# Kernel optimization log

Hardware: AMD Instinct MI355X
Metric: run time of the kernel (lower is better)

## Reference

```python
import jax, jax.numpy as jnp
import numpy as np

H = 128
N_ATOMS = 20000
N_BONDS = 60000
BATCH = 8


def _linear_params(key, fan_in, fan_out, bias=True):
    kw, kb = jax.random.split(key)
    lim = 1.0 / np.sqrt(fan_in)
    W = jax.random.uniform(kw, (fan_in, fan_out), jnp.float32, -lim, lim)
    if bias:
        b = jax.random.uniform(kb, (fan_out,), jnp.float32, -lim, lim)
        return W, b
    return W


def setup_inputs() -> dict:
    key = jax.random.key(0)
    ks = jax.random.split(key, 12)
    h = jax.random.normal(ks[0], (BATCH, N_ATOMS, H), jnp.float32)
    x = jax.random.normal(ks[1], (BATCH, N_ATOMS, 3), jnp.float32)
    bond_indices = jax.random.randint(ks[2], (N_BONDS, 2), 0, N_ATOMS, jnp.int64)
    Wm1, bm1 = _linear_params(ks[3], 2 * H + 1, H)
    Wm2, bm2 = _linear_params(ks[4], H, H)
    Wn1, bn1 = _linear_params(ks[5], 2 * H, H)
    Wn2, bn2 = _linear_params(ks[6], H, H)
    Wc1, bc1 = _linear_params(ks[7], H, H)
    # xavier_uniform gain=0.001 for final coord layer [1, H] in torch -> [H, 1] here
    lim = 0.001 * np.sqrt(6.0 / (H + 1))
    Wc2 = jax.random.uniform(ks[8], (H, 1), jnp.float32, -lim, lim)
    return dict(h=h, x=x, bond_indices=bond_indices,
                Wm1=Wm1, bm1=bm1, Wm2=Wm2, bm2=bm2,
                Wn1=Wn1, bn1=bn1, Wn2=Wn2, bn2=bn2,
                Wc1=Wc1, bc1=bc1, Wc2=Wc2)


def reference(h, x, bond_indices, Wm1, bm1, Wm2, bm2, Wn1, bn1, Wn2, bn2, Wc1, bc1, Wc2):
    silu = jax.nn.silu
    n_atoms = h.shape[1]
    src = bond_indices[:, 0]
    dst = bond_indices[:, 1]

    h_src = h[:, src, :]            # [B, E, H]
    h_dst = h[:, dst, :]
    coord_diff = x[:, dst, :] - x[:, src, :]   # [B, E, 3]
    dist = jnp.linalg.norm(coord_diff, axis=-1, keepdims=True)  # [B, E, 1]

    mi = jnp.concatenate([h_src, h_dst, dist], axis=-1)  # [B, E, 2H+1]
    messages = silu(silu(mi @ Wm1 + bm1) @ Wm2 + bm2)    # [B, E, H]

    aggregated = jnp.zeros_like(h).at[:, dst, :].add(messages).at[:, src, :].add(messages)

    h_in = jnp.concatenate([h, aggregated], axis=-1)     # [B, N, 2H]
    h_out = h + (silu(h_in @ Wn1 + bn1) @ Wn2 + bn2)

    coord_weights = silu(messages @ Wc1 + bc1) @ Wc2     # [B, E, 1]
    coord_diff_norm = coord_diff / (dist + 1e-8)
    upd = coord_diff_norm * coord_weights                # [B, E, 3]
    coord_update = jnp.zeros_like(x).at[:, dst, :].add(upd).at[:, src, :].add(-upd)

    ones = jnp.ones(src.shape[0], dtype=h.dtype)
    bond_counts = jnp.zeros(n_atoms, dtype=h.dtype).at[dst].add(ones).at[src].add(ones)
    bond_counts = jnp.clip(bond_counts, 1.0, None)
    x_out = x + coord_update / bond_counts[None, :, None]
    return h_out, x_out
```

## Files before the change

### kernel.cpp

```cpp
#include <hip/hip_runtime.h>


#define H      128
#define NA     20000
#define NB     60000
#define NBATCH 8
#define ADJ_CAP 32

typedef __bf16 bf16;
typedef __bf16 bf16x4 __attribute__((ext_vector_type(4)));
typedef __bf16 bf16x8 __attribute__((ext_vector_type(8)));
typedef float  f32x4  __attribute__((ext_vector_type(4)));

__device__ __forceinline__ float silu_f(float v) {
  float e = __expf(-v);
  return v * __builtin_amdgcn_rcpf(1.0f + e);
}

__device__ __forceinline__ int tswz(int row, int col) {
  return (row << 7) + (((((col) >> 3) ^ (row & 7)) << 3) | (col & 7));
}

__global__ void cast_h(const float* __restrict__ src, bf16* __restrict__ dst) {
  int i = blockIdx.x * 256 + threadIdx.x;
  float4 v = *(const float4*)(src + (size_t)i * 4);
  bf16x4 t = {(bf16)v.x, (bf16)v.y, (bf16)v.z, (bf16)v.w};
  *(bf16x4*)(dst + (size_t)i * 4) = t;
}

__device__ __forceinline__ void pack_one(const float* __restrict__ src,
                                         bf16* __restrict__ dst, int K,
                                         int i) {
  int k = i >> 7, n = i & 127;
  int nt = n >> 4, ks = k >> 5;
  int lane = (((k >> 3) & 3) << 4) | (n & 15);
  int j = k & 7;
  int KS = K >> 5;
  dst[((((nt * KS + ks) * 64) + lane) << 3) + j] = (bf16)src[i];
}

__global__ void pack_all(const float* __restrict__ Wm1,
                         const float* __restrict__ Wm2,
                         const float* __restrict__ Wn1,
                         const float* __restrict__ Wn2,
                         const float* __restrict__ Wc1,
                         bf16* __restrict__ W1p, bf16* __restrict__ W2p,
                         bf16* __restrict__ Wn1p, bf16* __restrict__ Wn2p,
                         bf16* __restrict__ Wc1p) {
  int i = blockIdx.x * 256 + threadIdx.x;
  if (i < 32768)       pack_one(Wm1, W1p, 256, i);
  else if (i < 49152)  pack_one(Wm2, W2p, 128, i - 32768);
  else if (i < 81920)  pack_one(Wn1, Wn1p, 256, i - 49152);
  else if (i < 98304)  pack_one(Wn2, Wn2p, 128, i - 81920);
  else if (i < 114688) pack_one(Wc1, Wc1p, 128, i - 98304);
}

__global__ void build_adj2(const int* __restrict__ bonds,
                           int* __restrict__ degI, int* __restrict__ adj2) {
  int e = blockIdx.x * 256 + threadIdx.x;
  if (e >= NB) return;
  int s = bonds[2 * e], d = bonds[2 * e + 1];
  int p = atomicAdd(&degI[s], 1);
  if (p < ADJ_CAP) adj2[s * ADJ_CAP + p] = (e << 1);
  p = atomicAdd(&degI[d], 1);
  if (p < ADJ_CAP) adj2[d * ADJ_CAP + p] = (e << 1) | 1;
}

__global__ __launch_bounds__(256, 4) void msg_kernel(
    const bf16* __restrict__ hb, const float* __restrict__ x,
    const int* __restrict__ bonds,
    const bf16* __restrict__ W1p, const float* __restrict__ bm1,
    const bf16* __restrict__ W2p, const float* __restrict__ bm2,
    const float* __restrict__ w1c,
    const bf16* __restrict__ Wc1p, const float* __restrict__ bc1,
    const float* __restrict__ Wc2,
    bf16* __restrict__ msgOut, float* __restrict__ updv) {
  __shared__ __align__(16) bf16 Tbuf[64 * 128];
  __shared__ __align__(16) float cds[64 * 3];
  __shared__ __align__(16) float dists[64];
  __shared__ __align__(16) float bm1s[128], bm2s[128], w1cs[128];
  __shared__ __align__(16) float bc1s[128], wc2s[128];
  __shared__ float cwpart[2][64];

  const int tid = threadIdx.x, blk = blockIdx.x;

  if (tid < 64) {
    int Rg = blk * 64 + tid;
    int bond = Rg >> 3, batch = Rg & 7;
    int s = bonds[2 * bond], dn = bonds[2 * bond + 1];
    const float* xs = x + (size_t)(batch * NA + s) * 3;
    const float* xd = x + (size_t)(batch * NA + dn) * 3;
    float c0 = xd[0] - xs[0], c1 = xd[1] - xs[1], c2 = xd[2] - xs[2];
    cds[tid * 3 + 0] = c0; cds[tid * 3 + 1] = c1; cds[tid * 3 + 2] = c2;
    dists[tid] = sqrtf(c0 * c0 + c1 * c1 + c2 * c2);
  }
  if (tid < 128) {
    bm1s[tid] = bm1[tid]; bm2s[tid] = bm2[tid]; w1cs[tid] = w1c[tid];
    bc1s[tid] = bc1[tid]; wc2s[tid] = Wc2[tid];
  }
  __syncthreads();

  const int lane = tid & 63;
  const int quad = lane >> 4, l16 = lane & 15;
  const int wave = tid >> 6;
  const int rowBase = (wave >> 1) * 32;
  const int colG = wave & 1;
  const int colBase = colG * 64;
  const bf16x8* W1v = (const bf16x8*)W1p;
  const bf16x8* W2v = (const bf16x8*)W2p;
  const bf16x8* Wc1v = (const bf16x8*)Wc1p;

  const int row0 = rowBase + l16, row1 = row0 + 16;
  const int Rg0 = blk * 64 + row0;
  const int bn0 = Rg0 >> 3, bat0 = Rg0 & 7;
  const bf16* hs0 = hb + (size_t)(bat0 * NA + bonds[2 * bn0]) * H;
  const bf16* hd0 = hb + (size_t)(bat0 * NA + bonds[2 * bn0 + 1]) * H;
  const int Rg1 = Rg0 + 16;
  const int bn1_ = Rg1 >> 3, bat1 = Rg1 & 7;
  const bf16* hs1 = hb + (size_t)(bat1 * NA + bonds[2 * bn1_]) * H;
  const bf16* hd1 = hb + (size_t)(bat1 * NA + bonds[2 * bn1_ + 1]) * H;
  const float dist0 = dists[row0], dist1 = dists[row1];

  f32x4 acc0[4], acc1[4];
#pragma unroll
  for (int nt = 0; nt < 4; nt++) {
    acc0[nt] = (f32x4){0.f, 0.f, 0.f, 0.f};
    acc1[nt] = (f32x4){0.f, 0.f, 0.f, 0.f};
  }

#pragma unroll
  for (int ks = 0; ks < 4; ks++) {
    bf16x8 a0 = *(const bf16x8*)(hs0 + ks * 32 + quad * 8);
    bf16x8 a1 = *(const bf16x8*)(hs1 + ks * 32 + quad * 8);
#pragma unroll
    for (int nt = 0; nt < 4; nt++) {
      bf16x8 b = W1v[((colG * 4 + nt) * 8 + ks) * 64 + lane];
      acc0[nt] = __builtin_amdgcn_mfma_f32_16x16x32_bf16(b, a0, acc0[nt], 0, 0, 0);
      acc1[nt] = __builtin_amdgcn_mfma_f32_16x16x32_bf16(b, a1, acc1[nt], 0, 0, 0);
    }
  }
#pragma unroll
  for (int ks = 4; ks < 8; ks++) {
    bf16x8 a0 = *(const bf16x8*)(hd0 + (ks - 4) * 32 + quad * 8);
    bf16x8 a1 = *(const bf16x8*)(hd1 + (ks - 4) * 32 + quad * 8);
#pragma unroll
    for (int nt = 0; nt < 4; nt++) {
      bf16x8 b = W1v[((colG * 4 + nt) * 8 + ks) * 64 + lane];
      acc0[nt] = __builtin_amdgcn_mfma_f32_16x16x32_bf16(b, a0, acc0[nt], 0, 0, 0);
      acc1[nt] = __builtin_amdgcn_mfma_f32_16x16x32_bf16(b, a1, acc1[nt], 0, 0, 0);
    }
  }
#pragma unroll
  for (int nt = 0; nt < 4; nt++) {
    int col = colBase + nt * 16 + quad * 4;
    f32x4 bb = *(const f32x4*)&bm1s[col];
    f32x4 wc = *(const f32x4*)&w1cs[col];
    bf16x4 o0, o1;
#pragma unroll
    for (int reg = 0; reg < 4; reg++) {
      o0[reg] = (bf16)silu_f(acc0[nt][reg] + bb[reg] + dist0 * wc[reg]);
      o1[reg] = (bf16)silu_f(acc1[nt][reg] + bb[reg] + dist1 * wc[reg]);
    }
    *(bf16x4*)&Tbuf[tswz(row0, col)] = o0;
    *(bf16x4*)&Tbuf[tswz(row1, col)] = o1;
  }
  __syncthreads();

#pragma unroll
  for (int nt = 0; nt < 4; nt++) {
    acc0[nt] = (f32x4){0.f, 0.f, 0.f, 0.f};
    acc1[nt] = (f32x4){0.f, 0.f, 0.f, 0.f};
  }
#pragma unroll
  for (int ks = 0; ks < 4; ks++) {
    bf16x8 a0 = *(const bf16x8*)&Tbuf[tswz(row0, ks * 32 + quad * 8)];
    bf16x8 a1 = *(const bf16x8*)&Tbuf[tswz(row1, ks * 32 + quad * 8)];
#pragma unroll
    for (int nt = 0; nt < 4; nt++) {
      bf16x8 b = W2v[((colG * 4 + nt) * 4 + ks) * 64 + lane];
      acc0[nt] = __builtin_amdgcn_mfma_f32_16x16x32_bf16(b, a0, acc0[nt], 0, 0, 0);
      acc1[nt] = __builtin_amdgcn_mfma_f32_16x16x32_bf16(b, a1, acc1[nt], 0, 0, 0);
    }
  }
  __syncthreads();
#pragma unroll
  for (int nt = 0; nt < 4; nt++) {
    int col = colBase + nt * 16 + quad * 4;
    f32x4 bb = *(const f32x4*)&bm2s[col];
    bf16x4 o0, o1;
#pragma unroll
    for (int reg = 0; reg < 4; reg++) {
      o0[reg] = (bf16)silu_f(acc0[nt][reg] + bb[reg]);
      o1[reg] = (bf16)silu_f(acc1[nt][reg] + bb[reg]);
    }
    *(bf16x4*)&Tbuf[tswz(row0, col)] = o0;
    *(bf16x4*)&Tbuf[tswz(row1, col)] = o1;
  }
  __syncthreads();

#pragma unroll
  for (int nt = 0; nt < 4; nt++) {
    acc0[nt] = (f32x4){0.f, 0.f, 0.f, 0.f};
    acc1[nt] = (f32x4){0.f, 0.f, 0.f, 0.f};
  }
#pragma unroll
  for (int ks = 0; ks < 4; ks++) {
    bf16x8 a0 = *(const bf16x8*)&Tbuf[tswz(row0, ks * 32 + quad * 8)];
    bf16x8 a1 = *(const bf16x8*)&Tbuf[tswz(row1, ks * 32 + quad * 8)];
#pragma unroll
    for (int nt = 0; nt < 4; nt++) {
      bf16x8 b = Wc1v[((colG * 4 + nt) * 4 + ks) * 64 + lane];
      acc0[nt] = __builtin_amdgcn_mfma_f32_16x16x32_bf16(b, a0, acc0[nt], 0, 0, 0);
      acc1[nt] = __builtin_amdgcn_mfma_f32_16x16x32_bf16(b, a1, acc1[nt], 0, 0, 0);
    }
  }

#pragma unroll
  for (int i = 0; i < 4; i++) {
    int item = i * 256 + tid;
    int row = item >> 4, cg = item & 15;
    *(bf16x8*)&msgOut[(size_t)(blk * 64 + row) * H + cg * 8] =
        *(const bf16x8*)&Tbuf[tswz(row, cg * 8)];
  }

  float s0 = 0.f, s1 = 0.f;
#pragma unroll
  for (int nt = 0; nt < 4; nt++) {
    int col = colBase + nt * 16 + quad * 4;
    f32x4 bb = *(const f32x4*)&bc1s[col];
    f32x4 w2 = *(const f32x4*)&wc2s[col];
#pragma unroll
    for (int reg = 0; reg < 4; reg++) {
      s0 += silu_f(acc0[nt][reg] + bb[reg]) * w2[reg];
      s1 += silu_f(acc1[nt][reg] + bb[reg]) * w2[reg];
    }
  }
  s0 += __shfl_xor(s0, 16); s0 += __shfl_xor(s0, 32);
  s1 += __shfl_xor(s1, 16); s1 += __shfl_xor(s1, 32);
  if (quad == 0) {
    cwpart[colG][row0] = s0;
    cwpart[colG][row1] = s1;
  }
  __syncthreads();
  if (colG == 0 && quad == 0) {
#pragma unroll
    for (int rs = 0; rs < 2; rs++) {
      int row = rs ? row1 : row0;
      size_t Rg = (size_t)blk * 64 + row;
      float cw = cwpart[0][row] + cwpart[1][row];
      float inv = 1.0f / (dists[row] + 1e-8f);
#pragma unroll
      for (int c = 0; c < 3; c++)
        updv[Rg * 3 + c] = cds[row * 3 + c] * inv * cw;
    }
  }
}

__global__ __launch_bounds__(256, 4) void node_kernel(
    const float* __restrict__ h, const bf16* __restrict__ hb,
    const bf16* __restrict__ msg, const float* __restrict__ updv,
    const int* __restrict__ degI, const int* __restrict__ adj2,
    const bf16* __restrict__ Wn1p, const float* __restrict__ bn1,
    const bf16* __restrict__ Wn2p, const float* __restrict__ bn2,
    const float* __restrict__ x,
    float* __restrict__ hout, float* __restrict__ xout) {
  __shared__ __align__(16) bf16 Abuf[64 * 128];
  __shared__ __align__(16) bf16 Tbuf[64 * 128];

  const int tid = threadIdx.x, blk = blockIdx.x;

  {
    const int row = tid >> 2, c4 = tid & 3;
    const int Rg = blk * 64 + row;
    const int atomA = Rg % NA, batA = Rg / NA;
    int deg = degI[atomA];
    if (deg > ADJ_CAP) deg = ADJ_CAP;
    const int* ap = adj2 + atomA * ADJ_CAP;
    float a32[32];
#pragma unroll
    for (int t = 0; t < 32; t++) a32[t] = 0.f;
    float sx = 0.f, sy = 0.f, sz = 0.f;
    int j = 0;
    for (; j + 2 <= deg; j += 2) {
      int2 e2 = *(const int2*)&ap[j];
      const bf16* m0 = msg + ((size_t)(e2.x >> 1) * 8 + batA) * H + c4 * 32;
      const bf16* m1 = msg + ((size_t)(e2.y >> 1) * 8 + batA) * H + c4 * 32;
      bf16x8 v0 = *(const bf16x8*)(m0),      v1 = *(const bf16x8*)(m0 + 8);
      bf16x8 v2 = *(const bf16x8*)(m0 + 16), v3 = *(const bf16x8*)(m0 + 24);
      bf16x8 u0 = *(const bf16x8*)(m1),      u1 = *(const bf16x8*)(m1 + 8);
      bf16x8 u2 = *(const bf16x8*)(m1 + 16), u3 = *(const bf16x8*)(m1 + 24);
      if (c4 == 0) {
        float sg0 = (e2.x & 1) ? 1.0f : -1.0f;
        float sg1 = (e2.y & 1) ? 1.0f : -1.0f;
        const float* uv0 = updv + ((size_t)(e2.x >> 1) * 8 + batA) * 3;
        const float* uv1 = updv + ((size_t)(e2.y >> 1) * 8 + batA) * 3;
        sx += sg0 * uv0[0] + sg1 * uv1[0];
        sy += sg0 * uv0[1] + sg1 * uv1[1];
        sz += sg0 * uv0[2] + sg1 * uv1[2];
      }
#pragma unroll
      for (int t = 0; t < 8; t++) {
        a32[t]      += (float)v0[t] + (float)u0[t];
        a32[8 + t]  += (float)v1[t] + (float)u1[t];
        a32[16 + t] += (float)v2[t] + (float)u2[t];
        a32[24 + t] += (float)v3[t] + (float)u3[t];
      }
    }
    if (j < deg) {
      int ent0 = ap[j];
      const bf16* m0 = msg + ((size_t)(ent0 >> 1) * 8 + batA) * H + c4 * 32;
      if (c4 == 0) {
        float sg0 = (ent0 & 1) ? 1.0f : -1.0f;
        const float* uv0 = updv + ((size_t)(ent0 >> 1) * 8 + batA) * 3;
        sx += sg0 * uv0[0]; sy += sg0 * uv0[1]; sz += sg0 * uv0[2];
      }
#pragma unroll
      for (int k = 0; k < 4; k++) {
        bf16x8 v = *(const bf16x8*)(m0 + 8 * k);
#pragma unroll
        for (int t = 0; t < 8; t++) a32[8 * k + t] += (float)v[t];
      }
    }
    if (c4 == 0) {
      float cnt = deg < 1 ? 1.0f : (float)deg;
      float inv = 1.0f / cnt;
      size_t o = (size_t)Rg * 3;
      xout[o + 0] = x[o + 0] + sx * inv;
      xout[o + 1] = x[o + 1] + sy * inv;
      xout[o + 2] = x[o + 2] + sz * inv;
    }
#pragma unroll
    for (int k = 0; k < 4; k++) {
      bf16x8 w;
#pragma unroll
      for (int t = 0; t < 8; t++) w[t] = (bf16)a32[8 * k + t];
      *(bf16x8*)&Abuf[tswz(row, c4 * 32 + 8 * k)] = w;
    }
  }
  __syncthreads();

  const int lane = tid & 63, wave = tid >> 6;
  const int quad = lane >> 4, l16 = lane & 15;
  const int rowBase = (wave >> 1) * 32, colG = wave & 1, colBase = colG * 64;
  const int row0 = rowBase + l16, row1 = row0 + 16;
  const size_t RgA0 = (size_t)blk * 64 + row0;
  const size_t RgA1 = RgA0 + 16;
  const bf16* hrow0 = hb + RgA0 * H;
  const bf16* hrow1 = hb + RgA1 * H;
  const bf16x8* W1v = (const bf16x8*)Wn1p;
  const bf16x8* W2v = (const bf16x8*)Wn2p;

  f32x4 acc0[4], acc1[4];
#pragma unroll
  for (int nt = 0; nt < 4; nt++) {
    acc0[nt] = (f32x4){0.f, 0.f, 0.f, 0.f};
    acc1[nt] = (f32x4){0.f, 0.f, 0.f, 0.f};
  }

#pragma unroll
  for (int ks = 0; ks < 4; ks++) {
    bf16x8 a0 = *(const bf16x8*)(hrow0 + ks * 32 + quad * 8);
    bf16x8 a1 = *(const bf16x8*)(hrow1 + ks * 32 + quad * 8);
#pragma unroll
    for (int nt = 0; nt < 4; nt++) {
      bf16x8 b = W1v[((colG * 4 + nt) * 8 + ks) * 64 + lane];
      acc0[nt] = __builtin_amdgcn_mfma_f32_16x16x32_bf16(b, a0, acc0[nt], 0, 0, 0);
      acc1[nt] = __builtin_amdgcn_mfma_f32_16x16x32_bf16(b, a1, acc1[nt], 0, 0, 0);
    }
  }
#pragma unroll
  for (int ks2 = 0; ks2 < 4; ks2++) {
    bf16x8 a0 = *(const bf16x8*)&Abuf[tswz(row0, ks2 * 32 + quad * 8)];
    bf16x8 a1 = *(const bf16x8*)&Abuf[tswz(row1, ks2 * 32 + quad * 8)];
#pragma unroll
    for (int nt = 0; nt < 4; nt++) {
      bf16x8 b = W1v[((colG * 4 + nt) * 8 + 4 + ks2) * 64 + lane];
      acc0[nt] = __builtin_amdgcn_mfma_f32_16x16x32_bf16(b, a0, acc0[nt], 0, 0, 0);
      acc1[nt] = __builtin_amdgcn_mfma_f32_16x16x32_bf16(b, a1, acc1[nt], 0, 0, 0);
    }
  }
#pragma unroll
  for (int nt = 0; nt < 4; nt++) {
    int col = colBase + nt * 16 + quad * 4;
    f32x4 bb = *(const f32x4*)&bn1[col];
    bf16x4 o0, o1;
#pragma unroll
    for (int reg = 0; reg < 4; reg++) {
      o0[reg] = (bf16)silu_f(acc0[nt][reg] + bb[reg]);
      o1[reg] = (bf16)silu_f(acc1[nt][reg] + bb[reg]);
    }
    *(bf16x4*)&Tbuf[tswz(row0, col)] = o0;
    *(bf16x4*)&Tbuf[tswz(row1, col)] = o1;
  }
  __syncthreads();

#pragma unroll
  for (int nt = 0; nt < 4; nt++) {
    acc0[nt] = (f32x4){0.f, 0.f, 0.f, 0.f};
    acc1[nt] = (f32x4){0.f, 0.f, 0.f, 0.f};
  }
#pragma unroll
  for (int ks = 0; ks < 4; ks++) {
    bf16x8 a0 = *(const bf16x8*)&Tbuf[tswz(row0, ks * 32 + quad * 8)];
    bf16x8 a1 = *(const bf16x8*)&Tbuf[tswz(row1, ks * 32 + quad * 8)];
#pragma unroll
    for (int nt = 0; nt < 4; nt++) {
      bf16x8 b = W2v[((colG * 4 + nt) * 4 + ks) * 64 + lane];
      acc0[nt] = __builtin_amdgcn_mfma_f32_16x16x32_bf16(b, a0, acc0[nt], 0, 0, 0);
      acc1[nt] = __builtin_amdgcn_mfma_f32_16x16x32_bf16(b, a1, acc1[nt], 0, 0, 0);
    }
  }
#pragma unroll
  for (int nt = 0; nt < 4; nt++) {
    int col = colBase + nt * 16 + quad * 4;
    f32x4 bb = *(const f32x4*)&bn2[col];
    f32x4 hv0 = *(const f32x4*)&h[RgA0 * H + col];
    f32x4 hv1 = *(const f32x4*)&h[RgA1 * H + col];
    f32x4 o0, o1;
#pragma unroll
    for (int reg = 0; reg < 4; reg++) {
      o0[reg] = hv0[reg] + acc0[nt][reg] + bb[reg];
      o1[reg] = hv1[reg] + acc1[nt][reg] + bb[reg];
    }
    *(f32x4*)&hout[RgA0 * H + col] = o0;
    *(f32x4*)&hout[RgA1 * H + col] = o1;
  }
}

extern "C" void kernel_launch(void* const* d_in, const int* in_sizes, int n_in,
                              void* d_out, int out_size, void* d_ws,
                              size_t ws_size, hipStream_t stream) {
  const float* h    = (const float*)d_in[0];
  const float* x    = (const float*)d_in[1];
  const int*  bonds = (const int*)d_in[2];
  const float* Wm1  = (const float*)d_in[3];
  const float* bm1  = (const float*)d_in[4];
  const float* Wm2  = (const float*)d_in[5];
  const float* bm2  = (const float*)d_in[6];
  const float* Wn1  = (const float*)d_in[7];
  const float* bn1  = (const float*)d_in[8];
  const float* Wn2  = (const float*)d_in[9];
  const float* bn2  = (const float*)d_in[10];
  const float* Wc1  = (const float*)d_in[11];
  const float* bc1  = (const float*)d_in[12];
  const float* Wc2  = (const float*)d_in[13];

  float* out  = (float*)d_out;
  float* hout = out;
  float* xout = out + (size_t)NBATCH * NA * H;

  char* ws = (char*)d_ws;
  const size_t OFF_DEG  = 0;
  const size_t OFF_W1   = 163840;
  const size_t OFF_W2   = OFF_W1 + 65536;
  const size_t OFF_WN1  = OFF_W2 + 32768;
  const size_t OFF_WN2  = OFF_WN1 + 65536;
  const size_t OFF_WC1  = OFF_WN2 + 32768;
  const size_t OFF_ADJ2 = 393216;
  const size_t OFF_UPDV = 2953216;
  const size_t OFF_HB   = 8713216;
  const size_t OFF_MSG  = 49673216;

  int*   degI = (int*)(ws + OFF_DEG);
  bf16*  W1p  = (bf16*)(ws + OFF_W1);
  bf16*  W2p  = (bf16*)(ws + OFF_W2);
  bf16*  Wn1p = (bf16*)(ws + OFF_WN1);
  bf16*  Wn2p = (bf16*)(ws + OFF_WN2);
  bf16*  Wc1p = (bf16*)(ws + OFF_WC1);
  int*   adj2 = (int*)(ws + OFF_ADJ2);
  float* updv = (float*)(ws + OFF_UPDV);
  bf16*  hb   = (bf16*)(ws + OFF_HB);
  bf16*  msgB = (bf16*)(ws + OFF_MSG);

  (void)hipMemsetAsync(degI, 0, NA * sizeof(int), stream);

  cast_h<<<NBATCH * NA * H / 1024, 256, 0, stream>>>(h, hb);
  pack_all<<<448, 256, 0, stream>>>(Wm1, Wm2, Wn1, Wn2, Wc1,
                                    W1p, W2p, Wn1p, Wn2p, Wc1p);
  build_adj2<<<(NB + 255) / 256, 256, 0, stream>>>(bonds, degI, adj2);

  msg_kernel<<<NB * NBATCH / 64, 256, 0, stream>>>(
      hb, x, bonds, W1p, bm1, W2p, bm2, Wm1 + 256 * H, Wc1p, bc1, Wc2,
      msgB, updv);
  node_kernel<<<NBATCH * NA / 64, 256, 0, stream>>>(
      h, hb, msgB, updv, degI, adj2, Wn1p, bn1, Wn2p, bn2, x,
      hout, xout);
}
```

Baseline: 433.0 us.

## Merge prep kernels into one launch and enlarge message tile to 96 rows

The three preprocessing kernels (cast h to bf16, pack weights, build adjacency) are fused into a single kernel that dispatches on block index, saving two launches. The message kernel now handles 96 edge-rows per block instead of 64, with each wave computing three 16-row MFMA fragments rather than two. This reuses each loaded weight fragment across more rows. In exchange it uses more accumulator registers and LDS, which may lower occupancy under the 4-blocks launch bound.

```diff
diff --git a/kernel.cpp b/kernel.cpp
--- a/kernel.cpp
+++ b/kernel.cpp
@@ -19,13 +19,6 @@
 
 __device__ __forceinline__ int tswz(int row, int col) {
   return (row << 7) + (((((col) >> 3) ^ (row & 7)) << 3) | (col & 7));
-}
-
-__global__ void cast_h(const float* __restrict__ src, bf16* __restrict__ dst) {
-  int i = blockIdx.x * 256 + threadIdx.x;
-  float4 v = *(const float4*)(src + (size_t)i * 4);
-  bf16x4 t = {(bf16)v.x, (bf16)v.y, (bf16)v.z, (bf16)v.w};
-  *(bf16x4*)(dst + (size_t)i * 4) = t;
 }
 
 __device__ __forceinline__ void pack_one(const float* __restrict__ src,
@@ -39,31 +32,43 @@
   dst[((((nt * KS + ks) * 64) + lane) << 3) + j] = (bf16)src[i];
 }
 
-__global__ void pack_all(const float* __restrict__ Wm1,
-                         const float* __restrict__ Wm2,
-                         const float* __restrict__ Wn1,
-                         const float* __restrict__ Wn2,
-                         const float* __restrict__ Wc1,
-                         bf16* __restrict__ W1p, bf16* __restrict__ W2p,
-                         bf16* __restrict__ Wn1p, bf16* __restrict__ Wn2p,
-                         bf16* __restrict__ Wc1p) {
-  int i = blockIdx.x * 256 + threadIdx.x;
-  if (i < 32768)       pack_one(Wm1, W1p, 256, i);
-  else if (i < 49152)  pack_one(Wm2, W2p, 128, i - 32768);
-  else if (i < 81920)  pack_one(Wn1, Wn1p, 256, i - 49152);
-  else if (i < 98304)  pack_one(Wn2, Wn2p, 128, i - 81920);
-  else if (i < 114688) pack_one(Wc1, Wc1p, 128, i - 98304);
-}
-
-__global__ void build_adj2(const int* __restrict__ bonds,
-                           int* __restrict__ degI, int* __restrict__ adj2) {
-  int e = blockIdx.x * 256 + threadIdx.x;
-  if (e >= NB) return;
-  int s = bonds[2 * e], d = bonds[2 * e + 1];
-  int p = atomicAdd(&degI[s], 1);
-  if (p < ADJ_CAP) adj2[s * ADJ_CAP + p] = (e << 1);
-  p = atomicAdd(&degI[d], 1);
-  if (p < ADJ_CAP) adj2[d * ADJ_CAP + p] = (e << 1) | 1;
+#define PREP_CAST_BLKS 20000
+#define PREP_PACK_BLKS 448
+#define PREP_ADJ_BLKS  235
+__global__ void prep_kernel(const float* __restrict__ h, bf16* __restrict__ hb,
+                            const float* __restrict__ Wm1,
+                            const float* __restrict__ Wm2,
+                            const float* __restrict__ Wn1,
+                            const float* __restrict__ Wn2,
+                            const float* __restrict__ Wc1,
+                            bf16* __restrict__ W1p, bf16* __restrict__ W2p,
+                            bf16* __restrict__ Wn1p, bf16* __restrict__ Wn2p,
+                            bf16* __restrict__ Wc1p,
+                            const int* __restrict__ bonds,
+                            int* __restrict__ degI, int* __restrict__ adj2) {
+  const int blk = blockIdx.x;
+  if (blk < PREP_CAST_BLKS) {
+    int i = blk * 256 + threadIdx.x;
+    float4 v = *(const float4*)(h + (size_t)i * 4);
+    bf16x4 t = {(bf16)v.x, (bf16)v.y, (bf16)v.z, (bf16)v.w};
+    *(bf16x4*)(hb + (size_t)i * 4) = t;
+  } else if (blk < PREP_CAST_BLKS + PREP_PACK_BLKS) {
+    int i = (blk - PREP_CAST_BLKS) * 256 + threadIdx.x;
+    if (i < 32768)       pack_one(Wm1, W1p, 256, i);
+    else if (i < 49152)  pack_one(Wm2, W2p, 128, i - 32768);
+    else if (i < 81920)  pack_one(Wn1, Wn1p, 256, i - 49152);
+    else if (i < 98304)  pack_one(Wn2, Wn2p, 128, i - 81920);
+    else if (i < 114688) pack_one(Wc1, Wc1p, 128, i - 98304);
+  } else {
+    int e = (blk - PREP_CAST_BLKS - PREP_PACK_BLKS) * 256 + threadIdx.x;
+    if (e < NB) {
+      int s = bonds[2 * e], d = bonds[2 * e + 1];
+      int p = atomicAdd(&degI[s], 1);
+      if (p < ADJ_CAP) adj2[s * ADJ_CAP + p] = (e << 1);
+      p = atomicAdd(&degI[d], 1);
+      if (p < ADJ_CAP) adj2[d * ADJ_CAP + p] = (e << 1) | 1;
+    }
+  }
 }
 
 __global__ __launch_bounds__(256, 4) void msg_kernel(
@@ -75,17 +80,17 @@
     const bf16* __restrict__ Wc1p, const float* __restrict__ bc1,
     const float* __restrict__ Wc2,
     bf16* __restrict__ msgOut, float* __restrict__ updv) {
-  __shared__ __align__(16) bf16 Tbuf[64 * 128];
-  __shared__ __align__(16) float cds[64 * 3];
-  __shared__ __align__(16) float dists[64];
+  __shared__ __align__(16) bf16 Tbuf[96 * 128];
+  __shared__ __align__(16) float cds[96 * 3];
+  __shared__ __align__(16) float dists[96];
   __shared__ __align__(16) float bm1s[128], bm2s[128], w1cs[128];
   __shared__ __align__(16) float bc1s[128], wc2s[128];
-  __shared__ float cwpart[2][64];
+  __shared__ float cwpart[2][96];
 
   const int tid = threadIdx.x, blk = blockIdx.x;
 
-  if (tid < 64) {
-    int Rg = blk * 64 + tid;
+  if (tid < 96) {
+    int Rg = blk * 96 + tid;
     int bond = Rg >> 3, batch = Rg & 7;
     int s = bonds[2 * bond], dn = bonds[2 * bond + 1];
     const float* xs = x + (size_t)(batch * NA + s) * 3;
@@ -103,15 +108,15 @@
   const int lane = tid & 63;
   const int quad = lane >> 4, l16 = lane & 15;
   const int wave = tid >> 6;
-  const int rowBase = (wave >> 1) * 32;
+  const int rowBase = (wave >> 1) * 48;
   const int colG = wave & 1;
   const int colBase = colG * 64;
   const bf16x8* W1v = (const bf16x8*)W1p;
   const bf16x8* W2v = (const bf16x8*)W2p;
   const bf16x8* Wc1v = (const bf16x8*)Wc1p;
 
-  const int row0 = rowBase + l16, row1 = row0 + 16;
-  const int Rg0 = blk * 64 + row0;
+  const int row0 = rowBase + l16, row1 = row0 + 16, row2 = row0 + 32;
+  const int Rg0 = blk * 96 + row0;
   const int bn0 = Rg0 >> 3, bat0 = Rg0 & 7;
   const bf16* hs0 = hb + (size_t)(bat0 * NA + bonds[2 * bn0]) * H;
   const bf16* hd0 = hb + (size_t)(bat0 * NA + bonds[2 * bn0 + 1]) * H;
@@ -119,35 +124,44 @@
   const int bn1_ = Rg1 >> 3, bat1 = Rg1 & 7;
   const bf16* hs1 = hb + (size_t)(bat1 * NA + bonds[2 * bn1_]) * H;
   const bf16* hd1 = hb + (size_t)(bat1 * NA + bonds[2 * bn1_ + 1]) * H;
-  const float dist0 = dists[row0], dist1 = dists[row1];
-
-  f32x4 acc0[4], acc1[4];
+  const int Rg2 = Rg0 + 32;
+  const int bn2_ = Rg2 >> 3, bat2 = Rg2 & 7;
+  const bf16* hs2 = hb + (size_t)(bat2 * NA + bonds[2 * bn2_]) * H;
+  const bf16* hd2 = hb + (size_t)(bat2 * NA + bonds[2 * bn2_ + 1]) * H;
+  const float dist0 = dists[row0], dist1 = dists[row1], dist2 = dists[row2];
+
+  f32x4 acc0[4], acc1[4], acc2[4];
 #pragma unroll
   for (int nt = 0; nt < 4; nt++) {
     acc0[nt] = (f32x4){0.f, 0.f, 0.f, 0.f};
     acc1[nt] = (f32x4){0.f, 0.f, 0.f, 0.f};
+    acc2[nt] = (f32x4){0.f, 0.f, 0.f, 0.f};
   }
 
 #pragma unroll
   for (int ks = 0; ks < 4; ks++) {
     bf16x8 a0 = *(const bf16x8*)(hs0 + ks * 32 + quad * 8);
     bf16x8 a1 = *(const bf16x8*)(hs1 + ks * 32 + quad * 8);
+    bf16x8 a2 = *(const bf16x8*)(hs2 + ks * 32 + quad * 8);
 #pragma unroll
     for (int nt = 0; nt < 4; nt++) {
       bf16x8 b = W1v[((colG * 4 + nt) * 8 + ks) * 64 + lane];
       acc0[nt] = __builtin_amdgcn_mfma_f32_16x16x32_bf16(b, a0, acc0[nt], 0, 0, 0);
       acc1[nt] = __builtin_amdgcn_mfma_f32_16x16x32_bf16(b, a1, acc1[nt], 0, 0, 0);
+      acc2[nt] = __builtin_amdgcn_mfma_f32_16x16x32_bf16(b, a2, acc2[nt], 0, 0, 0);
     }
   }
 #pragma unroll
   for (int ks = 4; ks < 8; ks++) {
     bf16x8 a0 = *(const bf16x8*)(hd0 + (ks - 4) * 32 + quad * 8);
     bf16x8 a1 = *(const bf16x8*)(hd1 + (ks - 4) * 32 + quad * 8);
+    bf16x8 a2 = *(const bf16x8*)(hd2 + (ks - 4) * 32 + quad * 8);
 #pragma unroll
     for (int nt = 0; nt < 4; nt++) {
       bf16x8 b = W1v[((colG * 4 + nt) * 8 + ks) * 64 + lane];
       acc0[nt] = __builtin_amdgcn_mfma_f32_16x16x32_bf16(b, a0, acc0[nt], 0, 0, 0);
       acc1[nt] = __builtin_amdgcn_mfma_f32_16x16x32_bf16(b, a1, acc1[nt], 0, 0, 0);
+      acc2[nt] = __builtin_amdgcn_mfma_f32_16x16x32_bf16(b, a2, acc2[nt], 0, 0, 0);
     }
   }
 #pragma unroll
@@ -155,14 +169,16 @@
     int col = colBase + nt * 16 + quad * 4;
     f32x4 bb = *(const f32x4*)&bm1s[col];
     f32x4 wc = *(const f32x4*)&w1cs[col];
-    bf16x4 o0, o1;
+    bf16x4 o0, o1, o2;
 #pragma unroll
     for (int reg = 0; reg < 4; reg++) {
       o0[reg] = (bf16)silu_f(acc0[nt][reg] + bb[reg] + dist0 * wc[reg]);
       o1[reg] = (bf16)silu_f(acc1[nt][reg] + bb[reg] + dist1 * wc[reg]);
+      o2[reg] = (bf16)silu_f(acc2[nt][reg] + bb[reg] + dist2 * wc[reg]);
     }
     *(bf16x4*)&Tbuf[tswz(row0, col)] = o0;
     *(bf16x4*)&Tbuf[tswz(row1, col)] = o1;
+    *(bf16x4*)&Tbuf[tswz(row2, col)] = o2;
   }
   __syncthreads();
 
@@ -170,16 +186,19 @@
   for (int nt = 0; nt < 4; nt++) {
     acc0[nt] = (f32x4){0.f, 0.f, 0.f, 0.f};
     acc1[nt] = (f32x4){0.f, 0.f, 0.f, 0.f};
+    acc2[nt] = (f32x4){0.f, 0.f, 0.f, 0.f};
   }
 #pragma unroll
   for (int ks = 0; ks < 4; ks++) {
     bf16x8 a0 = *(const bf16x8*)&Tbuf[tswz(row0, ks * 32 + quad * 8)];
     bf16x8 a1 = *(const bf16x8*)&Tbuf[tswz(row1, ks * 32 + quad * 8)];
+    bf16x8 a2 = *(const bf16x8*)&Tbuf[tswz(row2, ks * 32 + quad * 8)];
 #pragma unroll
     for (int nt = 0; nt < 4; nt++) {
       bf16x8 b = W2v[((colG * 4 + nt) * 4 + ks) * 64 + lane];
       acc0[nt] = __builtin_amdgcn_mfma_f32_16x16x32_bf16(b, a0, acc0[nt], 0, 0, 0);
       acc1[nt] = __builtin_amdgcn_mfma_f32_16x16x32_bf16(b, a1, acc1[nt], 0, 0, 0);
+      acc2[nt] = __builtin_amdgcn_mfma_f32_16x16x32_bf16(b, a2, acc2[nt], 0, 0, 0);
     }
   }
   __syncthreads();
@@ -187,14 +206,16 @@
   for (int nt = 0; nt < 4; nt++) {
     int col = colBase + nt * 16 + quad * 4;
     f32x4 bb = *(const f32x4*)&bm2s[col];
-    bf16x4 o0, o1;
+    bf16x4 o0, o1, o2;
 #pragma unroll
     for (int reg = 0; reg < 4; reg++) {
       o0[reg] = (bf16)silu_f(acc0[nt][reg] + bb[reg]);
       o1[reg] = (bf16)silu_f(acc1[nt][reg] + bb[reg]);
+      o2[reg] = (bf16)silu_f(acc2[nt][reg] + bb[reg]);
     }
     *(bf16x4*)&Tbuf[tswz(row0, col)] = o0;
     *(bf16x4*)&Tbuf[tswz(row1, col)] = o1;
+    *(bf16x4*)&Tbuf[tswz(row2, col)] = o2;
   }
   __syncthreads();
 
@@ -202,28 +223,31 @@
   for (int nt = 0; nt < 4; nt++) {
     acc0[nt] = (f32x4){0.f, 0.f, 0.f, 0.f};
     acc1[nt] = (f32x4){0.f, 0.f, 0.f, 0.f};
+    acc2[nt] = (f32x4){0.f, 0.f, 0.f, 0.f};
   }
 #pragma unroll
   for (int ks = 0; ks < 4; ks++) {
     bf16x8 a0 = *(const bf16x8*)&Tbuf[tswz(row0, ks * 32 + quad * 8)];
     bf16x8 a1 = *(const bf16x8*)&Tbuf[tswz(row1, ks * 32 + quad * 8)];
+    bf16x8 a2 = *(const bf16x8*)&Tbuf[tswz(row2, ks * 32 + quad * 8)];
 #pragma unroll
     for (int nt = 0; nt < 4; nt++) {
       bf16x8 b = Wc1v[((colG * 4 + nt) * 4 + ks) * 64 + lane];
       acc0[nt] = __builtin_amdgcn_mfma_f32_16x16x32_bf16(b, a0, acc0[nt], 0, 0, 0);
       acc1[nt] = __builtin_amdgcn_mfma_f32_16x16x32_bf16(b, a1, acc1[nt], 0, 0, 0);
-    }
-  }
-
-#pragma unroll
-  for (int i = 0; i < 4; i++) {
+      acc2[nt] = __builtin_amdgcn_mfma_f32_16x16x32_bf16(b, a2, acc2[nt], 0, 0, 0);
+    }
+  }
+
+#pragma unroll
+  for (int i = 0; i < 6; i++) {
     int item = i * 256 + tid;
     int row = item >> 4, cg = item & 15;
-    *(bf16x8*)&msgOut[(size_t)(blk * 64 + row) * H + cg * 8] =
+    *(bf16x8*)&msgOut[(size_t)(blk * 96 + row) * H + cg * 8] =
         *(const bf16x8*)&Tbuf[tswz(row, cg * 8)];
   }
 
-  float s0 = 0.f, s1 = 0.f;
+  float s0 = 0.f, s1 = 0.f, s2 = 0.f;
 #pragma unroll
   for (int nt = 0; nt < 4; nt++) {
     int col = colBase + nt * 16 + quad * 4;
@@ -233,20 +257,23 @@
     for (int reg = 0; reg < 4; reg++) {
       s0 += silu_f(acc0[nt][reg] + bb[reg]) * w2[reg];
       s1 += silu_f(acc1[nt][reg] + bb[reg]) * w2[reg];
+      s2 += silu_f(acc2[nt][reg] + bb[reg]) * w2[reg];
     }
   }
   s0 += __shfl_xor(s0, 16); s0 += __shfl_xor(s0, 32);
   s1 += __shfl_xor(s1, 16); s1 += __shfl_xor(s1, 32);
+  s2 += __shfl_xor(s2, 16); s2 += __shfl_xor(s2, 32);
   if (quad == 0) {
     cwpart[colG][row0] = s0;
     cwpart[colG][row1] = s1;
+    cwpart[colG][row2] = s2;
   }
   __syncthreads();
   if (colG == 0 && quad == 0) {
 #pragma unroll
-    for (int rs = 0; rs < 2; rs++) {
-      int row = rs ? row1 : row0;
-      size_t Rg = (size_t)blk * 64 + row;
+    for (int rs = 0; rs < 3; rs++) {
+      int row = row0 + rs * 16;
+      size_t Rg = (size_t)blk * 96 + row;
       float cw = cwpart[0][row] + cwpart[1][row];
       float inv = 1.0f / (dists[row] + 1e-8f);
 #pragma unroll
@@ -474,12 +501,11 @@
 
   (void)hipMemsetAsync(degI, 0, NA * sizeof(int), stream);
 
-  cast_h<<<NBATCH * NA * H / 1024, 256, 0, stream>>>(h, hb);
-  pack_all<<<448, 256, 0, stream>>>(Wm1, Wm2, Wn1, Wn2, Wc1,
-                                    W1p, W2p, Wn1p, Wn2p, Wc1p);
-  build_adj2<<<(NB + 255) / 256, 256, 0, stream>>>(bonds, degI, adj2);
-
-  msg_kernel<<<NB * NBATCH / 64, 256, 0, stream>>>(
+  prep_kernel<<<PREP_CAST_BLKS + PREP_PACK_BLKS + PREP_ADJ_BLKS, 256, 0,
+                stream>>>(h, hb, Wm1, Wm2, Wn1, Wn2, Wc1,
+                          W1p, W2p, Wn1p, Wn2p, Wc1p, bonds, degI, adj2);
+
+  msg_kernel<<<NB * NBATCH / 96, 256, 0, stream>>>(
       hb, x, bonds, W1p, bm1, W2p, bm2, Wm1 + 256 * H, Wc1p, bc1, Wc2,
       msgB, updv);
   node_kernel<<<NBATCH * NA / 64, 256, 0, stream>>>(
```

Result: no change. 432.2 us (-0.2%).
